# Optimization experiments

Hardware: AMD Instinct MI355X
Metric: run time of the kernel (lower is better)

The kernel has to match this reference:

```python
import jax, jax.numpy as jnp
import numpy as np

B, S, CC, CF, E, H, NH = 16, 1024, 8, 8, 64, 1024, 16
DH = H // NH
VOCAB = 10000
EPS = 1e-5


def layer_norm(x, g, b):
    m = x.mean(-1, keepdims=True)
    v = x.var(-1, keepdims=True)
    return (x - m) / jnp.sqrt(v + EPS) * g + b


def setup_inputs():
    key = jax.random.key(0)
    ks = jax.random.split(key, 30)
    f32 = jnp.float32
    n = lambda k, shp, s=0.02: jax.random.normal(k, shp, f32) * s
    inp = {}
    inp['cate_x'] = jax.random.randint(ks[0], (B, S, CC), 0, VOCAB)
    inp['cont_x'] = jax.random.normal(ks[1], (B, S, CF), f32)
    inp['mask'] = jax.random.randint(ks[2], (B, S), 0, 2)
    # parameters
    inp['emb_table'] = n(ks[3], (VOCAB, E)).at[0].set(0.0)  # padding_idx=0
    inp['cate_W'] = n(ks[4], (CC * E, H)); inp['cate_b'] = jnp.zeros((H,), f32)
    inp['cate_ln_g'] = jnp.ones((H,), f32); inp['cate_ln_b'] = jnp.zeros((H,), f32)
    inp['bn_g'] = jnp.ones((CF,), f32); inp['bn_b'] = jnp.zeros((CF,), f32)
    inp['cont_W'] = n(ks[5], (CF, H)); inp['cont_b'] = jnp.zeros((H,), f32)
    inp['cont_ln_g'] = jnp.ones((H,), f32); inp['cont_ln_b'] = jnp.zeros((H,), f32)
    inp['comb_W'] = n(ks[6], (2 * H, H)); inp['comb_b'] = jnp.zeros((H,), f32)
    inp['comb_ln_g'] = jnp.ones((H,), f32); inp['comb_ln_b'] = jnp.zeros((H,), f32)
    inp['Wq'] = n(ks[7], (H, H)); inp['bq'] = jnp.zeros((H,), f32)
    inp['Wk'] = n(ks[8], (H, H)); inp['bk'] = jnp.zeros((H,), f32)
    inp['Wv'] = n(ks[9], (H, H)); inp['bv'] = jnp.zeros((H,), f32)
    inp['Wo'] = n(ks[10], (H, H)); inp['bo'] = jnp.zeros((H,), f32)
    return inp


def reference(cate_x, cont_x, mask, emb_table, cate_W, cate_b, cate_ln_g, cate_ln_b,
              bn_g, bn_b, cont_W, cont_b, cont_ln_g, cont_ln_b,
              comb_W, comb_b, comb_ln_g, comb_ln_b,
              Wq, bq, Wk, bk, Wv, bv, Wo, bo):
    # categorical path: embed -> flatten cols -> Linear+LN
    cate_emb = emb_table[cate_x].reshape(B, S, CC * E)
    cate_h = layer_norm(cate_emb @ cate_W + cate_b, cate_ln_g, cate_ln_b)
    # continuous path: BatchNorm1d over flattened (B*S, CF) with batch stats
    xf = cont_x.reshape(-1, CF)
    mu = xf.mean(0)
    var = xf.var(0)  # biased, as torch BN normalization
    xn = ((xf - mu) / jnp.sqrt(var + EPS) * bn_g + bn_b).reshape(B, S, CF)
    cont_h = layer_norm(xn @ cont_W + cont_b, cont_ln_g, cont_ln_b)
    # combine: ReLU -> Linear -> LN
    seq = jax.nn.relu(jnp.concatenate([cate_h, cont_h], axis=2))
    x = layer_norm(seq @ comb_W + comb_b, comb_ln_g, comb_ln_b)  # [B,S,H]
    # multi-head attention (dropout is identity in eval)
    Q = (x @ Wq + bq).reshape(B, S, NH, DH)
    K = (x @ Wk + bk).reshape(B, S, NH, DH)
    V = (x @ Wv + bv).reshape(B, S, NH, DH)
    scores = jnp.einsum('bqhd,bkhd->bhqk', Q, K) / np.sqrt(DH).astype(np.float32)
    # faithful to source: mask broadcast over the QUERY axis
    scores = jnp.where(mask[:, None, :, None] == 0, -1e7, scores)
    attn = jax.nn.softmax(scores, axis=-1)
    out = jnp.einsum('bhqk,bkhd->bqhd', attn, V).reshape(B, S, H)
    out = out @ Wo + bo
    return out[:, -1:, -1]  # [B,1]
```

## Files before the change

kernel.cpp:

```cpp
#include <hip/hip_runtime.h>
#include <hip/hip_bf16.h>
#include <math.h>

#define EPS 1e-5f

typedef unsigned short u16;
typedef __attribute__((ext_vector_type(8))) short bf16x8;
typedef __attribute__((ext_vector_type(4))) float f32x4;

__device__ __forceinline__ float b2f(u16 u) {
  union { unsigned int i; float f; } v; v.i = ((unsigned int)u) << 16; return v.f;
}
__device__ __forceinline__ u16 f2b(float f) {
  union { float f; unsigned int i; } v; v.f = f;
  unsigned int r = v.i + 0x7fff + ((v.i >> 16) & 1);
  return (u16)(r >> 16);
}

__device__ __forceinline__ void gload_lds16(const u16* g, u16* l) {
  __builtin_amdgcn_global_load_lds(
      (const __attribute__((address_space(1))) unsigned int*)g,
      (__attribute__((address_space(3))) unsigned int*)l, 16, 0, 0);
}

__global__ __launch_bounds__(256) void prep_k(
    const float* __restrict__ cx, float* __restrict__ part_bn,
    float* __restrict__ out, float* __restrict__ Sall,
    const float* __restrict__ emb, u16* __restrict__ embb,
    const float* __restrict__ cate_W, u16* __restrict__ cateWT) {
  __shared__ float shmem[64 * 65];
  const int bid = blockIdx.x, tid = threadIdx.x;

  if (bid == 0) {
    if (tid < 16) out[tid] = 0.f;
    for (int i = tid; i < 544; i += 256) Sall[i] = 0.f;
    return;
  }
  if (bid <= 64) {
    int pb = bid - 1;
    int gid = pb * 256 + tid;
    float4 a = ((const float4*)cx)[2 * gid];
    float4 b = ((const float4*)cx)[2 * gid + 1];
    float v[16];
    v[0] = a.x; v[1] = a.y; v[2] = a.z; v[3] = a.w;
    v[4] = b.x; v[5] = b.y; v[6] = b.z; v[7] = b.w;
#pragma unroll
    for (int i = 0; i < 8; ++i) v[8 + i] = v[i] * v[i];
#pragma unroll
    for (int off = 32; off; off >>= 1)
#pragma unroll
      for (int i = 0; i < 16; ++i) v[i] += __shfl_down(v[i], off);
    int l = tid & 63, wv_ = tid >> 6;
    if (l == 0)
#pragma unroll
      for (int i = 0; i < 16; ++i) shmem[wv_ * 16 + i] = v[i];
    __syncthreads();
    if (tid < 16)
      part_bn[pb * 16 + tid] = shmem[tid] + shmem[16 + tid] + shmem[32 + tid] + shmem[48 + tid];
    return;
  }
  if (bid <= 689) {
    int i = (bid - 65) * 256 + tid;
    if (i < 160000) {
      float4 v = ((const float4*)emb)[i];
      ushort4 u; u.x = f2b(v.x); u.y = f2b(v.y); u.z = f2b(v.z); u.w = f2b(v.w);
      ((ushort4*)embb)[i] = u;
    }
    return;
  }
  {
    int local = bid - 690;
    int n0 = (local & 15) * 64, k0 = (local >> 4) * 64;
    int c = tid & 63, r0 = tid >> 6;
#pragma unroll
    for (int i = 0; i < 16; ++i) {
      int r = r0 + i * 4;
      shmem[r * 65 + c] = cate_W[(size_t)(k0 + r) * 1024 + n0 + c];
    }
    __syncthreads();
#pragma unroll
    for (int i = 0; i < 16; ++i) {
      int r = r0 + i * 4;
      cateWT[(size_t)(n0 + r) * 512 + k0 + c] = f2b(shmem[c * 65 + r]);
    }
  }
}

template <int MODE>
__global__ __launch_bounds__(512) void gemm256(
    const u16* __restrict__ A0, const u16* __restrict__ A1,
    const int* __restrict__ idx, const u16* __restrict__ embb,
    const u16* __restrict__ BT, const float* __restrict__ bias,
    u16* __restrict__ C, int K) {
  __shared__ u16 As[2][2][8192];
  __shared__ u16 Bs[2][2][8192];
  __shared__ int sidx[MODE == 1 ? 2048 : 4];
  const int tid = threadIdx.x;
  const int bid = blockIdx.x;
  const int chunk = gridDim.x >> 3;
  const int swz = (bid & 7) * chunk + (bid >> 3);
  const int row0 = (swz >> 2) * 256;
  const int col0 = (swz & 3) * 256;

  const int rr8 = tid >> 3;
  const int p8  = tid & 7;
  const int sl  = p8 ^ (rr8 & 7);

  const int l   = tid & 63;
  const int w   = tid >> 6;
  const int wrh = w >> 2;
  const int wcq = w & 3;
  const int hb  = wcq >> 1;
  const int rbb = (wcq & 1) * 64;
  const int lr  = l & 15;
  const int lk  = l >> 4;

  f32x4 acc[8][4];
#pragma unroll
  for (int m = 0; m < 8; ++m)
#pragma unroll
    for (int n = 0; n < 4; ++n) acc[m][n] = (f32x4){0.f, 0.f, 0.f, 0.f};

  const int nt = K >> 6;
  const int nit = nt >> 1;

  if (MODE == 1) {
    *(int4*)&sidx[tid * 4] = *(const int4*)&idx[row0 * 8 + tid * 4];
    __syncthreads();
  }

  auto stageA = [&](int t, int h) {
    const int k0 = t << 6;
    const int buf = t & 1;
#pragma unroll
    for (int i = 0; i < 2; ++i) {
      const u16* asrc;
      if (MODE == 1) {
        int id = sidx[(h * 128 + i * 64 + rr8) * 8 + (k0 >> 6)];
        asrc = embb + (size_t)id * 64 + sl * 8;
      } else {
        int ar = row0 + h * 128 + i * 64 + rr8;
        const u16* base = (k0 < 1024) ? A0 : A1;
        asrc = base + (size_t)ar * 1024 + (k0 & 1023) + sl * 8;
      }
      gload_lds16(asrc, &As[buf][h][i * 4096 + tid * 8]);
    }
  };
  auto stageB = [&](int t, int h) {
    const int k0 = t << 6;
    const int buf = t & 1;
#pragma unroll
    for (int i = 0; i < 2; ++i) {
      int br = col0 + h * 128 + i * 64 + rr8;
      gload_lds16(BT + (size_t)br * K + k0 + sl * 8,
                  &Bs[buf][h][i * 4096 + tid * 8]);
    }
  };

  bf16x8 bfr[4][2];
  auto loadB = [&](int buf) {
#pragma unroll
    for (int n = 0; n < 4; ++n)
#pragma unroll
      for (int ks = 0; ks < 2; ++ks) {
        int rowb = rbb + n * 16 + lr;
        int ph = (ks * 4 + lk) ^ (lr & 7);
        bfr[n][ks] = *(const bf16x8*)&Bs[buf][hb][rowb * 64 + ph * 8];
      }
  };
  auto loadA = [&](bf16x8 (&af)[2][2], int buf, int q) {
#pragma unroll
    for (int mm = 0; mm < 2; ++mm)
#pragma unroll
      for (int ks = 0; ks < 2; ++ks) {
        int rowa = (q * 2 + mm) * 16 + lr;
        int ph = (ks * 4 + lk) ^ (lr & 7);
        af[mm][ks] = *(const bf16x8*)&As[buf][wrh][rowa * 64 + ph * 8];
      }
  };
  auto mfma_quad = [&](bf16x8 (&af)[2][2], int q) {
    __builtin_amdgcn_s_setprio(1);
#pragma unroll
    for (int ks = 0; ks < 2; ++ks)
#pragma unroll
      for (int mm = 0; mm < 2; ++mm)
#pragma unroll
        for (int n = 0; n < 4; ++n)
          acc[q * 2 + mm][n] = __builtin_amdgcn_mfma_f32_16x16x32_bf16(
              af[mm][ks], bfr[n][ks], acc[q * 2 + mm][n], 0, 0, 0);
    __builtin_amdgcn_s_setprio(0);
  };

  stageA(0, 0); stageA(0, 1);
  stageB(0, 0); stageB(0, 1);
  stageB(1, 0); stageB(1, 1);
  asm volatile("s_waitcnt vmcnt(4)" ::: "memory");
  __builtin_amdgcn_s_barrier();

  for (int it = 0; it < nit; ++it) {
    const int T = it * 2;
    const bool more = (T + 2 < nt);
    bf16x8 af[2][2];

    loadB(0); loadA(af, 0, 0);
    stageA(T + 1, 0);
    __builtin_amdgcn_s_barrier();
    asm volatile("s_waitcnt lgkmcnt(0)" ::: "memory");
    mfma_quad(af, 0);
    __builtin_amdgcn_s_barrier();
    loadA(af, 0, 1);
    stageA(T + 1, 1);
    __builtin_amdgcn_s_barrier();
    asm volatile("s_waitcnt lgkmcnt(0)" ::: "memory");
    mfma_quad(af, 1);
    __builtin_amdgcn_s_barrier();
    loadA(af, 0, 2);
    if (more) stageB(T + 2, 0);
    __builtin_amdgcn_s_barrier();
    asm volatile("s_waitcnt lgkmcnt(0)" ::: "memory");
    mfma_quad(af, 2);
    __builtin_amdgcn_s_barrier();
    loadA(af, 0, 3);
    if (more) stageB(T + 2, 1);
    __builtin_amdgcn_s_barrier();
    asm volatile("s_waitcnt lgkmcnt(0)" ::: "memory");
    mfma_quad(af, 3);
    if (more) asm volatile("s_waitcnt vmcnt(4)" ::: "memory");
    else      asm volatile("s_waitcnt vmcnt(0)" ::: "memory");
    __builtin_amdgcn_s_barrier();

    loadB(1); loadA(af, 1, 0);
    if (more) stageA(T + 2, 0);
    __builtin_amdgcn_s_barrier();
    asm volatile("s_waitcnt lgkmcnt(0)" ::: "memory");
    mfma_quad(af, 0);
    __builtin_amdgcn_s_barrier();
    loadA(af, 1, 1);
    if (more) stageA(T + 2, 1);
    __builtin_amdgcn_s_barrier();
    asm volatile("s_waitcnt lgkmcnt(0)" ::: "memory");
    mfma_quad(af, 1);
    __builtin_amdgcn_s_barrier();
    loadA(af, 1, 2);
    if (more) stageB(T + 3, 0);
    __builtin_amdgcn_s_barrier();
    asm volatile("s_waitcnt lgkmcnt(0)" ::: "memory");
    mfma_quad(af, 2);
    __builtin_amdgcn_s_barrier();
    loadA(af, 1, 3);
    if (more) stageB(T + 3, 1);
    __builtin_amdgcn_s_barrier();
    asm volatile("s_waitcnt lgkmcnt(0)" ::: "memory");
    mfma_quad(af, 3);
    if (it + 1 < nit) {
      asm volatile("s_waitcnt vmcnt(4)" ::: "memory");
      __builtin_amdgcn_s_barrier();
    }
  }

  float bv_[4];
#pragma unroll
  for (int n = 0; n < 4; ++n) bv_[n] = bias[col0 + wcq * 64 + n * 16 + lr];
#pragma unroll
  for (int m = 0; m < 8; ++m) {
#pragma unroll
    for (int n = 0; n < 4; ++n) {
      int cc = col0 + wcq * 64 + n * 16 + lr;
#pragma unroll
      for (int q4 = 0; q4 < 4; ++q4) {
        int rr = row0 + wrh * 128 + m * 16 + lk * 4 + q4;
        C[(size_t)rr * 1024 + cc] = f2b(acc[m][n][q4] + bv_[n]);
      }
    }
  }
}

__device__ __forceinline__ void ln_body(u16* __restrict__ buf,
                                        const float* __restrict__ g,
                                        const float* __restrict__ b, int relu,
                                        int blk, int tid) {
  int lane = tid & 63, wave = tid >> 6;
  size_t row = (size_t)blk * 4 + wave;
  u16* p = buf + row * 1024 + lane * 16;
  uint4 u0 = *(uint4*)p;
  uint4 u1 = *(uint4*)(p + 8);
  float x[16];
#pragma unroll
  for (int i = 0; i < 4; ++i) {
    unsigned int w0 = ((unsigned int*)&u0)[i];
    unsigned int w1 = ((unsigned int*)&u1)[i];
    x[2 * i]     = b2f((u16)(w0 & 0xffff));
    x[2 * i + 1] = b2f((u16)(w0 >> 16));
    x[8 + 2 * i]     = b2f((u16)(w1 & 0xffff));
    x[8 + 2 * i + 1] = b2f((u16)(w1 >> 16));
  }
  float s = 0.f, s2 = 0.f;
#pragma unroll
  for (int i = 0; i < 16; ++i) { s += x[i]; s2 += x[i] * x[i]; }
#pragma unroll
  for (int off = 32; off; off >>= 1) { s += __shfl_xor(s, off); s2 += __shfl_xor(s2, off); }
  float mean = s * (1.f / 1024.f);
  float var = s2 * (1.f / 1024.f) - mean * mean;
  float rs = rsqrtf(var + EPS);
  float y[16];
#pragma unroll
  for (int q = 0; q < 4; ++q) {
    float4 gv = *(const float4*)(g + lane * 16 + q * 4);
    float4 bv = *(const float4*)(b + lane * 16 + q * 4);
    y[4 * q]     = (x[4 * q]     - mean) * rs * gv.x + bv.x;
    y[4 * q + 1] = (x[4 * q + 1] - mean) * rs * gv.y + bv.y;
    y[4 * q + 2] = (x[4 * q + 2] - mean) * rs * gv.z + bv.z;
    y[4 * q + 3] = (x[4 * q + 3] - mean) * rs * gv.w + bv.w;
  }
  if (relu)
#pragma unroll
    for (int i = 0; i < 16; ++i) y[i] = fmaxf(y[i], 0.f);
  uint4 o0, o1;
#pragma unroll
  for (int i = 0; i < 4; ++i) {
    ((unsigned int*)&o0)[i] = (unsigned int)f2b(y[2 * i]) | ((unsigned int)f2b(y[2 * i + 1]) << 16);
    ((unsigned int*)&o1)[i] = (unsigned int)f2b(y[8 + 2 * i]) | ((unsigned int)f2b(y[8 + 2 * i + 1]) << 16);
  }
  *(uint4*)p = o0;
  *(uint4*)(p + 8) = o1;
}

__device__ __forceinline__ void cont_body(const float* __restrict__ cx,
                                          const float* __restrict__ part_bn,
                                          const float* __restrict__ bn_g,
                                          const float* __restrict__ bn_b,
                                          const float* __restrict__ W,
                                          const float* __restrict__ cb,
                                          const float* __restrict__ g,
                                          const float* __restrict__ bb,
                                          u16* __restrict__ out,
                                          int row0, int tid) {
  __shared__ float sp[4][16];
  __shared__ float tt[16];
  __shared__ float ab[2][8];
  __shared__ float xn[8][8];
  __shared__ float rr1[4][8], rr2[4][8];

  if (tid < 64) {
    int f = tid & 15, qd = tid >> 4;
    float s = 0.f;
    for (int j = qd * 16; j < qd * 16 + 16; ++j) s += part_bn[j * 16 + f];
    sp[qd][f] = s;
  }
  __syncthreads();
  if (tid < 16) tt[tid] = sp[0][tid] + sp[1][tid] + sp[2][tid] + sp[3][tid];
  __syncthreads();
  if (tid < 8) {
    float mu = tt[tid] * (1.f / 16384.f);
    float var = tt[8 + tid] * (1.f / 16384.f) - mu * mu;
    float a = rsqrtf(var + EPS) * bn_g[tid];
    ab[0][tid] = a;
    ab[1][tid] = bn_b[tid] - mu * a;
  }
  __syncthreads();
  if (tid < 64) {
    int r = tid >> 3, f = tid & 7;
    xn[r][f] = ab[0][f] * cx[(row0 + r) * 8 + f] + ab[1][f];
  }
  __syncthreads();

  int c = tid * 4;
  float4 cbv = *(const float4*)(cb + c);
  float acc[8][4];
#pragma unroll
  for (int r = 0; r < 8; ++r) {
    acc[r][0] = cbv.x; acc[r][1] = cbv.y; acc[r][2] = cbv.z; acc[r][3] = cbv.w;
  }
  for (int k = 0; k < 8; ++k) {
    float4 w4 = *(const float4*)(W + k * 1024 + c);
#pragma unroll
    for (int r = 0; r < 8; ++r) {
      float xv = xn[r][k];
      acc[r][0] = fmaf(xv, w4.x, acc[r][0]);
      acc[r][1] = fmaf(xv, w4.y, acc[r][1]);
      acc[r][2] = fmaf(xv, w4.z, acc[r][2]);
      acc[r][3] = fmaf(xv, w4.w, acc[r][3]);
    }
  }
  float s1[8], s2[8];
#pragma unroll
  for (int r = 0; r < 8; ++r) {
    s1[r] = acc[r][0] + acc[r][1] + acc[r][2] + acc[r][3];
    s2[r] = acc[r][0] * acc[r][0] + acc[r][1] * acc[r][1] +
            acc[r][2] * acc[r][2] + acc[r][3] * acc[r][3];
  }
#pragma unroll
  for (int off = 32; off; off >>= 1)
#pragma unroll
    for (int r = 0; r < 8; ++r) {
      s1[r] += __shfl_down(s1[r], off);
      s2[r] += __shfl_down(s2[r], off);
    }
  int lane = tid & 63, wv = tid >> 6;
  if (lane == 0)
#pragma unroll
    for (int r = 0; r < 8; ++r) { rr1[wv][r] = s1[r]; rr2[wv][r] = s2[r]; }
  __syncthreads();
  float4 gv = *(const float4*)(g + c);
  float4 bv = *(const float4*)(bb + c);
#pragma unroll
  for (int r = 0; r < 8; ++r) {
    float ss = rr1[0][r] + rr1[1][r] + rr1[2][r] + rr1[3][r];
    float qq = rr2[0][r] + rr2[1][r] + rr2[2][r] + rr2[3][r];
    float mean = ss * (1.f / 1024.f);
    float var = qq * (1.f / 1024.f) - mean * mean;
    float rs = rsqrtf(var + EPS);
    float y0 = fmaxf((acc[r][0] - mean) * rs * gv.x + bv.x, 0.f);
    float y1 = fmaxf((acc[r][1] - mean) * rs * gv.y + bv.y, 0.f);
    float y2 = fmaxf((acc[r][2] - mean) * rs * gv.z + bv.z, 0.f);
    float y3 = fmaxf((acc[r][3] - mean) * rs * gv.w + bv.w, 0.f);
    ushort4 o; o.x = f2b(y0); o.y = f2b(y1); o.z = f2b(y2); o.w = f2b(y3);
    *(ushort4*)(out + (size_t)(row0 + r) * 1024 + c) = o;
  }
}

__global__ __launch_bounds__(256) void mid_k(
    u16* __restrict__ X1, const float* __restrict__ cate_g,
    const float* __restrict__ cate_bb,
    const float* __restrict__ comb_W, u16* __restrict__ combWT,
    const float* __restrict__ Wv, const float* __restrict__ Wo,
    const float* __restrict__ comb_g, const float* __restrict__ comb_bbv,
    u16* __restrict__ wvob_hi, u16* __restrict__ wvob_lo,
    float* __restrict__ Swg, float* __restrict__ Swb,
    const float* __restrict__ bv, const float* __restrict__ bo,
    float* __restrict__ bc,
    const float* __restrict__ cx, const float* __restrict__ part_bn,
    const float* __restrict__ bn_g, const float* __restrict__ bn_b,
    const float* __restrict__ cont_W, const float* __restrict__ cont_b,
    const float* __restrict__ cont_g, const float* __restrict__ cont_bb,
    u16* __restrict__ X2) {
  __shared__ float shmem[64 * 65];
  const int bid = blockIdx.x, tid = threadIdx.x;
  if (bid < 4096) {
    ln_body(X1, cate_g, cate_bb, 1, bid, tid);
    return;
  }
  if (bid < 4608) {
    int local = bid - 4096;
    int n0 = (local & 15) * 64, k0 = (local >> 4) * 64;
    int c = tid & 63, r0 = tid >> 6;
#pragma unroll
    for (int i = 0; i < 16; ++i) {
      int r = r0 + i * 4;
      shmem[r * 65 + c] = comb_W[(size_t)(k0 + r) * 1024 + n0 + c];
    }
    __syncthreads();
#pragma unroll
    for (int i = 0; i < 16; ++i) {
      int r = r0 + i * 4;
      combWT[(size_t)(n0 + r) * 2048 + k0 + c] = f2b(shmem[c * 65 + r]);
    }
    return;
  }
  if (bid < 4672) {
    int local = bid - 4608;
    int h = local >> 2, jc = local & 3;
    if (tid < 64) shmem[tid] = Wo[(size_t)(h * 64 + tid) * 1024 + 1023];
    __syncthreads();
    int j = jc * 256 + tid;
    const float* vr = Wv + (size_t)j * 1024 + h * 64;
    float s = 0.f;
    for (int d4 = 0; d4 < 64; d4 += 4) {
      float4 w4 = *(const float4*)(vr + d4);
      s = fmaf(w4.x, shmem[d4], s);
      s = fmaf(w4.y, shmem[d4 + 1], s);
      s = fmaf(w4.z, shmem[d4 + 2], s);
      s = fmaf(w4.w, shmem[d4 + 3], s);
    }
    float sg_ = s * comb_g[j];
    u16 hi = f2b(sg_);
    float lo = sg_ - b2f(hi);
    wvob_hi[h * 1024 + j] = hi;
    wvob_lo[h * 1024 + j] = f2b(lo);
    float swgp = sg_;
    float swbp = s * comb_bbv[j];
#pragma unroll
    for (int off = 32; off; off >>= 1) {
      swgp += __shfl_down(swgp, off);
      swbp += __shfl_down(swbp, off);
    }
    int lane = tid & 63, wv = tid >> 6;
    if (lane == 0) { shmem[64 + wv] = swgp; shmem[68 + wv] = swbp; }
    __syncthreads();
    if (tid == 0) {
      atomicAdd(&Swg[h], shmem[64] + shmem[65] + shmem[66] + shmem[67]);
      atomicAdd(&Swb[h], shmem[68] + shmem[69] + shmem[70] + shmem[71]);
    }
    return;
  }
  if (bid < 6720) {
    int row0 = (bid - 4672) * 8;
    cont_body(cx, part_bn, bn_g, bn_b, cont_W, cont_b, cont_g, cont_bb, X2,
              row0, tid);
    return;
  }
  {
    float s = 0.f;
    for (int i = tid; i < 1024; i += 256)
      s = fmaf(bv[i], Wo[(size_t)i * 1024 + 1023], s);
#pragma unroll
    for (int off = 32; off; off >>= 1) s += __shfl_down(s, off);
    int lane = tid & 63, wv = tid >> 6;
    if (lane == 0) shmem[wv] = s;
    __syncthreads();
    if (tid == 0) bc[0] = shmem[0] + shmem[1] + shmem[2] + shmem[3] + bo[1023];
  }
}

__global__ __launch_bounds__(256) void qproj_k(const u16* __restrict__ x,
                                               const float* __restrict__ g,
                                               const float* __restrict__ bb,
                                               const float* __restrict__ Wq,
                                               const float* __restrict__ bq,
                                               float* __restrict__ qpart) {
  __shared__ u16 xs[16][1024];
  __shared__ float part[16][16][16];
  __shared__ float ps1[16][16], ps2[16][16];
  __shared__ float sm[16], sr[16];
  int tid = threadIdx.x;
  int cb = blockIdx.x >> 2, kq4 = blockIdx.x & 3;
  for (int i = tid; i < 4096; i += 256) {
    int b = i >> 8, off = (i & 255) * 4;
    *(ushort4*)&xs[b][off] =
        *(const ushort4*)(x + ((size_t)(b * 1024 + 1023)) * 1024 + off);
  }
  __syncthreads();
  {
    int b = tid >> 4, seg = tid & 15;
    float s = 0.f, s2 = 0.f;
    for (int k = seg * 64; k < seg * 64 + 64; ++k) {
      float v = b2f(xs[b][k]);
      s += v;
      s2 = fmaf(v, v, s2);
    }
    ps1[b][seg] = s;
    ps2[b][seg] = s2;
  }
  __syncthreads();
  if (tid < 16) {
    float s = 0.f, s2 = 0.f;
#pragma unroll
    for (int j = 0; j < 16; ++j) { s += ps1[tid][j]; s2 += ps2[tid][j]; }
    float mean = s * (1.f / 1024.f);
    float var = s2 * (1.f / 1024.f) - mean * mean;
    sm[tid] = mean;
    sr[tid] = rsqrtf(var + EPS);
  }
  __syncthreads();
  for (int i = tid; i < 4096; i += 256) {
    int b = i >> 8, off = (i & 255) * 4;
    ushort4 u = *(ushort4*)&xs[b][off];
    float4 gv = *(const float4*)(g + off);
    float4 bvv = *(const float4*)(bb + off);
    float m = sm[b], r = sr[b];
    ushort4 o;
    o.x = f2b((b2f(u.x) - m) * r * gv.x + bvv.x);
    o.y = f2b((b2f(u.y) - m) * r * gv.y + bvv.y);
    o.z = f2b((b2f(u.z) - m) * r * gv.z + bvv.z);
    o.w = f2b((b2f(u.w) - m) * r * gv.w + bvv.w);
    *(ushort4*)&xs[b][off] = o;
  }
  __syncthreads();
  int c = tid & 15;
  int col = cb * 16 + c;
  int kq = tid >> 4;
  float acc[16];
#pragma unroll
  for (int b = 0; b < 16; ++b) acc[b] = 0.f;
  int kbase = kq4 * 256 + kq * 16;
  for (int k = kbase; k < kbase + 16; ++k) {
    float wv = Wq[(size_t)k * 1024 + col];
#pragma unroll
    for (int b = 0; b < 16; ++b) acc[b] = fmaf(b2f(xs[b][k]), wv, acc[b]);
  }
#pragma unroll
  for (int b = 0; b < 16; ++b) part[kq][b][c] = acc[b];
  __syncthreads();
  {
    int b = tid >> 4, cc = tid & 15;
    float s = 0.f;
#pragma unroll
    for (int j = 0; j < 16; ++j) s += part[j][b][cc];
    if (kq4 == 0) s += bq[cb * 16 + cc];
    qpart[kq4 * 16384 + b * 1024 + cb * 16 + cc] = s;
  }
}

__global__ __launch_bounds__(256) void kq_k(const float* __restrict__ Wk,
                                            const float* __restrict__ bk,
                                            const float* __restrict__ qpart,
                                            const float* __restrict__ g,
                                            const float* __restrict__ bb,
                                            u16* __restrict__ qtb,
                                            float* __restrict__ bkq,
                                            float* __restrict__ Sg,
                                            float* __restrict__ Sb) {
  int h = blockIdx.x >> 2, jc = blockIdx.x & 3;
  int tid = threadIdx.x;
  __shared__ float Qs[16][64];
  __shared__ float rg[4][16], rb[4][16];
  for (int i = tid; i < 1024; i += 256) {
    int b = i >> 6, d = i & 63;
    int o = b * 1024 + h * 64 + d;
    Qs[b][d] = qpart[o] + qpart[16384 + o] + qpart[32768 + o] + qpart[49152 + o];
  }
  __syncthreads();
  int j = jc * 256 + tid;
  float acc[16];
#pragma unroll
  for (int b = 0; b < 16; ++b) acc[b] = 0.f;
  const float* wr = Wk + (size_t)j * 1024 + h * 64;
  for (int d4 = 0; d4 < 64; d4 += 4) {
    float4 w4 = *(const float4*)(wr + d4);
#pragma unroll
    for (int b = 0; b < 16; ++b) {
      acc[b] = fmaf(w4.x, Qs[b][d4], acc[b]);
      acc[b] = fmaf(w4.y, Qs[b][d4 + 1], acc[b]);
      acc[b] = fmaf(w4.z, Qs[b][d4 + 2], acc[b]);
      acc[b] = fmaf(w4.w, Qs[b][d4 + 3], acc[b]);
    }
  }
  float gj = g[j], bbj = bb[j];
  float sgp[16], sbp[16];
#pragma unroll
  for (int b = 0; b < 16; ++b) {
    u16 qg = f2b(acc[b] * gj);
    qtb[((size_t)b * 16 + h) * 1024 + j] = qg;
    sgp[b] = b2f(qg);
    sbp[b] = acc[b] * bbj;
  }
#pragma unroll
  for (int off = 32; off; off >>= 1)
#pragma unroll
    for (int b = 0; b < 16; ++b) {
      sgp[b] += __shfl_down(sgp[b], off);
      sbp[b] += __shfl_down(sbp[b], off);
    }
  int lane = tid & 63, wv = tid >> 6;
  if (lane == 0)
#pragma unroll
    for (int b = 0; b < 16; ++b) { rg[wv][b] = sgp[b]; rb[wv][b] = sbp[b]; }
  __syncthreads();
  if (tid < 16) {
    int b = tid;
    atomicAdd(&Sg[b * 16 + h], rg[0][b] + rg[1][b] + rg[2][b] + rg[3][b]);
    atomicAdd(&Sb[b * 16 + h], rb[0][b] + rb[1][b] + rb[2][b] + rb[3][b]);
  }
  if (jc == 0 && tid < 16) {
    int b = tid;
    float s = 0.f;
    for (int d = 0; d < 64; ++d) s = fmaf(bk[h * 64 + d], Qs[b][d], s);
    bkq[b * 16 + h] = s;
  }
}

__global__ __launch_bounds__(256) void score_k(
    const u16* __restrict__ x, const u16* __restrict__ qtb,
    const float* __restrict__ bkq, const int* __restrict__ mask,
    const u16* __restrict__ whi, const u16* __restrict__ wlo,
    const float* __restrict__ Sg, const float* __restrict__ Sb,
    const float* __restrict__ Swg, const float* __restrict__ Swb,
    float* __restrict__ sc, float* __restrict__ y) {
  int b = blockIdx.x >> 6, kg = blockIdx.x & 63;
  int tid = threadIdx.x;
  int l = tid & 63, w = tid >> 6;
  int keybase = kg * 16;
  int lr = l & 15, ls = l >> 4;
  int masked = (mask[b * 1024 + 1023] == 0);

  bf16x8 ones;
#pragma unroll
  for (int j = 0; j < 8; ++j) ones[j] = (short)0x3F80;

  f32x4 acc = (f32x4){0.f, 0.f, 0.f, 0.f};
  f32x4 acy = (f32x4){0.f, 0.f, 0.f, 0.f};
  f32x4 as1 = (f32x4){0.f, 0.f, 0.f, 0.f};
  f32x4 as2 = (f32x4){0.f, 0.f, 0.f, 0.f};
  const u16* xb = x + (size_t)b * 1024 * 1024;
  const u16* qb = qtb + (size_t)b * 16 * 1024;
  const int k0beg = w * 256;
  for (int k0 = k0beg; k0 < k0beg + 256; k0 += 32) {
    bf16x8 bfr = *(const bf16x8*)&qb[(size_t)lr * 1024 + k0 + ls * 8];
    bf16x8 bh  = *(const bf16x8*)&whi[(size_t)lr * 1024 + k0 + ls * 8];
    bf16x8 bl  = *(const bf16x8*)&wlo[(size_t)lr * 1024 + k0 + ls * 8];
    bf16x8 afr = *(const bf16x8*)&xb[(size_t)(keybase + lr) * 1024 + k0 + ls * 8];
    acc = __builtin_amdgcn_mfma_f32_16x16x32_bf16(afr, bfr, acc, 0, 0, 0);
    acy = __builtin_amdgcn_mfma_f32_16x16x32_bf16(afr, bh, acy, 0, 0, 0);
    acy = __builtin_amdgcn_mfma_f32_16x16x32_bf16(afr, bl, acy, 0, 0, 0);
    as1 = __builtin_amdgcn_mfma_f32_16x16x32_bf16(afr, ones, as1, 0, 0, 0);
    as2 = __builtin_amdgcn_mfma_f32_16x16x32_bf16(afr, afr, as2, 0, 0, 0);
  }

  __shared__ float red[3][64][16];
  if (w > 0) {
    float* r = red[w - 1][l];
#pragma unroll
    for (int q = 0; q < 4; ++q) {
      r[q] = acc[q]; r[4 + q] = acy[q]; r[8 + q] = as1[q]; r[12 + q] = as2[q];
    }
  }
  __syncthreads();
  if (w == 0) {
#pragma unroll
    for (int i = 0; i < 3; ++i) {
      const float* r = red[i][l];
#pragma unroll
      for (int q = 0; q < 4; ++q) {
        acc[q] += r[q]; acy[q] += r[4 + q]; as1[q] += r[8 + q]; as2[q] += r[12 + q];
      }
    }
    int h = lr;
    float bq_  = bkq[b * 16 + h];
    float Sgv  = Sg[b * 16 + h];
    float Sbv  = Sb[b * 16 + h];
    float Swgv = Swg[h];
    float Swbv = Swb[h];
#pragma unroll
    for (int q = 0; q < 4; ++q) {
      int key = keybase + ls * 4 + q;
      float s1 = as1[q];
      float s2 = __shfl(as2[q], ls * 4 + q + 16 * ls);
      float mean = s1 * (1.f / 1024.f);
      float var  = s2 * (1.f / 1024.f) - mean * mean;
      float rs   = rsqrtf(var + EPS);
      float sraw = rs * acc[q] - rs * mean * Sgv + Sbv + bq_;
      float v = masked ? 0.f : sraw * 0.125f;
      sc[((size_t)b * 16 + h) * 1024 + key] = v;
      y[((size_t)b * 16 + h) * 1024 + key] =
          rs * acy[q] - rs * mean * Swgv + Swbv;
    }
  }
}

__global__ __launch_bounds__(256) void fin_k(const float* __restrict__ sc,
                                             const float* __restrict__ y,
                                             const float* __restrict__ bc,
                                             float* __restrict__ out) {
  int bh = blockIdx.x, tid = threadIdx.x;
  float4 v = ((const float4*)(sc + (size_t)bh * 1024))[tid];
  float m = fmaxf(fmaxf(v.x, v.y), fmaxf(v.z, v.w));
#pragma unroll
  for (int off = 32; off; off >>= 1) m = fmaxf(m, __shfl_down(m, off));
  __shared__ float rm[4], rs_[4], rd_[4];
  int lane = tid & 63, wv = tid >> 6;
  if (lane == 0) rm[wv] = m;
  __syncthreads();
  m = fmaxf(fmaxf(rm[0], rm[1]), fmaxf(rm[2], rm[3]));
  float e0 = expf(v.x - m), e1 = expf(v.y - m), e2 = expf(v.z - m), e3 = expf(v.w - m);
  float4 yv = ((const float4*)(y + (size_t)bh * 1024))[tid];
  float s = e0 + e1 + e2 + e3;
  float d = e0 * yv.x + e1 * yv.y + e2 * yv.z + e3 * yv.w;
#pragma unroll
  for (int off = 32; off; off >>= 1) {
    s += __shfl_down(s, off);
    d += __shfl_down(d, off);
  }
  if (lane == 0) { rs_[wv] = s; rd_[wv] = d; }
  __syncthreads();
  if (tid == 0) {
    float Z = rs_[0] + rs_[1] + rs_[2] + rs_[3];
    float D = rd_[0] + rd_[1] + rd_[2] + rd_[3];
    float add = D / Z;
    if ((bh & 15) == 0) add += bc[0];
    atomicAdd(&out[bh >> 4], add);
  }
}

extern "C" void kernel_launch(void* const* d_in, const int* in_sizes, int n_in,
                              void* d_out, int out_size, void* d_ws, size_t ws_size,
                              hipStream_t stream) {
  const int*   cate_x  = (const int*)d_in[0];
  const float* cont_x  = (const float*)d_in[1];
  const int*   mask    = (const int*)d_in[2];
  const float* emb     = (const float*)d_in[3];
  const float* cate_W  = (const float*)d_in[4];
  const float* cate_b  = (const float*)d_in[5];
  const float* cate_g  = (const float*)d_in[6];
  const float* cate_bb = (const float*)d_in[7];
  const float* bn_g    = (const float*)d_in[8];
  const float* bn_b    = (const float*)d_in[9];
  const float* cont_W  = (const float*)d_in[10];
  const float* cont_b  = (const float*)d_in[11];
  const float* cont_g  = (const float*)d_in[12];
  const float* cont_bb = (const float*)d_in[13];
  const float* Wq = (const float*)d_in[18]; const float* bq = (const float*)d_in[19];
  const float* Wk = (const float*)d_in[20]; const float* bk = (const float*)d_in[21];
  const float* Wv = (const float*)d_in[22]; const float* bv = (const float*)d_in[23];
  const float* Wo = (const float*)d_in[24]; const float* bo = (const float*)d_in[25];
  const float* comb_W  = (const float*)d_in[14];
  const float* comb_b  = (const float*)d_in[15];
  const float* comb_g  = (const float*)d_in[16];
  const float* comb_bb = (const float*)d_in[17];
  float* out = (float*)d_out;

  char* w = (char*)d_ws;
  float* part_bn = (float*)(w + 256);
  u16* embb      = (u16*)(w + 131328);
  u16* cateWT    = (u16*)(w + 1411328);
  u16* combWT    = (u16*)(w + 2459904);
  float* sc      = (float*)(w + 6654208);
  u16*   qtb     = (u16*)(w + 7702784);
  float* bkq     = (float*)(w + 8292608);
  float* ybuf    = (float*)(w + 8388608);
  u16* wvob_hi   = (u16*)(w + 9437184);
  u16* wvob_lo   = (u16*)(w + 9469952);
  float* qpart   = (float*)(w + 9506816);
  float* Sall    = (float*)(w + 10162176);
  float* Sg      = Sall;
  float* Sb      = Sall + 256;
  float* Swg     = Sall + 512;
  float* Swb     = Sall + 528;
  float* bc      = Sall + 552;
  u16* X1        = (u16*)(w + 10848512);
  u16* X2        = X1 + (size_t)16777216;
  u16* xb        = X2 + (size_t)16777216;

  prep_k<<<818, 256, 0, stream>>>(cont_x, part_bn, out, Sall, emb, embb,
                                  cate_W, cateWT);

  gemm256<1><<<256, 512, 0, stream>>>(nullptr, nullptr, cate_x, embb, cateWT,
                                      cate_b, X1, 512);
  mid_k<<<6721, 256, 0, stream>>>(X1, cate_g, cate_bb, comb_W, combWT, Wv, Wo,
                                  comb_g, comb_bb, wvob_hi, wvob_lo, Swg, Swb,
                                  bv, bo, bc, cont_x, part_bn, bn_g, bn_b,
                                  cont_W, cont_b, cont_g, cont_bb, X2);
  gemm256<2><<<256, 512, 0, stream>>>(X1, X2, nullptr, nullptr, combWT,
                                      comb_b, xb, 2048);

  qproj_k<<<256, 256, 0, stream>>>(xb, comb_g, comb_bb, Wq, bq, qpart);
  kq_k<<<64, 256, 0, stream>>>(Wk, bk, qpart, comb_g, comb_bb, qtb, bkq, Sg, Sb);
  score_k<<<1024, 256, 0, stream>>>(xb, qtb, bkq, mask, wvob_hi, wvob_lo,
                                    Sg, Sb, Swg, Swb, sc, ybuf);
  fin_k<<<256, 256, 0, stream>>>(sc, ybuf, bc, out);
}
```

Before: 181.5 us.

## Pre-gather embeddings into dense bf16 matrix before categorical GEMM

Replaces whole-table bf16 conversion and in-GEMM indexed gather with a separate kernel that gathers and converts the embedding rows for every token into a dense A matrix stored in the X2 buffer. The categorical GEMM then loads A contiguously instead of via shared-memory indices. This makes GEMM loads regular but adds a large extra write and read of the gathered activations in place of reading a small cached table.

```diff
diff --git a/kernel.cpp b/kernel.cpp
--- a/kernel.cpp
+++ b/kernel.cpp
@@ -23,10 +23,27 @@
       (__attribute__((address_space(3))) unsigned int*)l, 16, 0, 0);
 }
 
+__global__ __launch_bounds__(256) void gather_k(const int* __restrict__ idx,
+                                                const float* __restrict__ emb,
+                                                u16* __restrict__ Agath) {
+  int tid = threadIdx.x;
+  int p = blockIdx.x * 32 + (tid >> 3);
+  int q = tid & 7;
+  int id = idx[p];
+  const float* src = emb + (size_t)id * 64 + q * 8;
+  float4 a = *(const float4*)src;
+  float4 b = *(const float4*)(src + 4);
+  uint4 o;
+  o.x = (unsigned int)f2b(a.x) | ((unsigned int)f2b(a.y) << 16);
+  o.y = (unsigned int)f2b(a.z) | ((unsigned int)f2b(a.w) << 16);
+  o.z = (unsigned int)f2b(b.x) | ((unsigned int)f2b(b.y) << 16);
+  o.w = (unsigned int)f2b(b.z) | ((unsigned int)f2b(b.w) << 16);
+  *(uint4*)(Agath + (size_t)p * 64 + q * 8) = o;
+}
+
 __global__ __launch_bounds__(256) void prep_k(
     const float* __restrict__ cx, float* __restrict__ part_bn,
     float* __restrict__ out, float* __restrict__ Sall,
-    const float* __restrict__ emb, u16* __restrict__ embb,
     const float* __restrict__ cate_W, u16* __restrict__ cateWT) {
   __shared__ float shmem[64 * 65];
   const int bid = blockIdx.x, tid = threadIdx.x;
@@ -59,17 +76,8 @@
       part_bn[pb * 16 + tid] = shmem[tid] + shmem[16 + tid] + shmem[32 + tid] + shmem[48 + tid];
     return;
   }
-  if (bid <= 689) {
-    int i = (bid - 65) * 256 + tid;
-    if (i < 160000) {
-      float4 v = ((const float4*)emb)[i];
-      ushort4 u; u.x = f2b(v.x); u.y = f2b(v.y); u.z = f2b(v.z); u.w = f2b(v.w);
-      ((ushort4*)embb)[i] = u;
-    }
-    return;
-  }
   {
-    int local = bid - 690;
+    int local = bid - 65;
     int n0 = (local & 15) * 64, k0 = (local >> 4) * 64;
     int c = tid & 63, r0 = tid >> 6;
 #pragma unroll
@@ -89,12 +97,10 @@
 template <int MODE>
 __global__ __launch_bounds__(512) void gemm256(
     const u16* __restrict__ A0, const u16* __restrict__ A1,
-    const int* __restrict__ idx, const u16* __restrict__ embb,
     const u16* __restrict__ BT, const float* __restrict__ bias,
     u16* __restrict__ C, int K) {
   __shared__ u16 As[2][2][8192];
   __shared__ u16 Bs[2][2][8192];
-  __shared__ int sidx[MODE == 1 ? 2048 : 4];
   const int tid = threadIdx.x;
   const int bid = blockIdx.x;
   const int chunk = gridDim.x >> 3;
@@ -124,22 +130,16 @@
   const int nt = K >> 6;
   const int nit = nt >> 1;
 
-  if (MODE == 1) {
-    *(int4*)&sidx[tid * 4] = *(const int4*)&idx[row0 * 8 + tid * 4];
-    __syncthreads();
-  }
-
   auto stageA = [&](int t, int h) {
     const int k0 = t << 6;
     const int buf = t & 1;
 #pragma unroll
     for (int i = 0; i < 2; ++i) {
+      int ar = row0 + h * 128 + i * 64 + rr8;
       const u16* asrc;
       if (MODE == 1) {
-        int id = sidx[(h * 128 + i * 64 + rr8) * 8 + (k0 >> 6)];
-        asrc = embb + (size_t)id * 64 + sl * 8;
+        asrc = A0 + (size_t)ar * 512 + k0 + sl * 8;
       } else {
-        int ar = row0 + h * 128 + i * 64 + rr8;
         const u16* base = (k0 < 1024) ? A0 : A1;
         asrc = base + (size_t)ar * 1024 + (k0 & 1023) + sl * 8;
       }
@@ -800,7 +800,6 @@
 
   char* w = (char*)d_ws;
   float* part_bn = (float*)(w + 256);
-  u16* embb      = (u16*)(w + 131328);
   u16* cateWT    = (u16*)(w + 1411328);
   u16* combWT    = (u16*)(w + 2459904);
   float* sc      = (float*)(w + 6654208);
@@ -819,18 +818,17 @@
   u16* X1        = (u16*)(w + 10848512);
   u16* X2        = X1 + (size_t)16777216;
   u16* xb        = X2 + (size_t)16777216;
-
-  prep_k<<<818, 256, 0, stream>>>(cont_x, part_bn, out, Sall, emb, embb,
-                                  cate_W, cateWT);
-
-  gemm256<1><<<256, 512, 0, stream>>>(nullptr, nullptr, cate_x, embb, cateWT,
-                                      cate_b, X1, 512);
+  u16* Agath     = X2;
+
+  gather_k<<<4096, 256, 0, stream>>>(cate_x, emb, Agath);
+  prep_k<<<193, 256, 0, stream>>>(cont_x, part_bn, out, Sall, cate_W, cateWT);
+
+  gemm256<1><<<256, 512, 0, stream>>>(Agath, nullptr, cateWT, cate_b, X1, 512);
   mid_k<<<6721, 256, 0, stream>>>(X1, cate_g, cate_bb, comb_W, combWT, Wv, Wo,
                                   comb_g, comb_bb, wvob_hi, wvob_lo, Swg, Swb,
                                   bv, bo, bc, cont_x, part_bn, bn_g, bn_b,
                                   cont_W, cont_b, cont_g, cont_bb, X2);
-  gemm256<2><<<256, 512, 0, stream>>>(X1, X2, nullptr, nullptr, combWT,
-                                      comb_b, xb, 2048);
+  gemm256<2><<<256, 512, 0, stream>>>(X1, X2, combWT, comb_b, xb, 2048);
 
   qproj_k<<<256, 256, 0, stream>>>(xb, comb_g, comb_bb, Wq, bq, qpart);
   kq_k<<<64, 256, 0, stream>>>(Wk, bk, qpart, comb_g, comb_bb, qtb, bkq, Sg, Sb);
```

After: 185.7 us. 2.3% more time.

## Fuse last-token Q projection and K-fold kernels into one launch

Applied to the files above, without the earlier changes.

Merges qproj_k and kq_k into a single qk_k kernel. Each of the 64 blocks (one head, one column quarter) computes the head's 64 Q columns over all of K and reduces the four partial sums in shared memory, so the qpart buffer round trip and one kernel launch go away. In exchange each head's Q slice is recomputed by 4 blocks, and the grid falls from 256 to 64 blocks, each running a longer serial 256-step K loop per thread. That lowers parallelism and adds redundant Wq reads.

```diff
diff --git a/kernel.cpp b/kernel.cpp
--- a/kernel.cpp
+++ b/kernel.cpp
@@ -512,18 +512,26 @@
   }
 }
 
-__global__ __launch_bounds__(256) void qproj_k(const u16* __restrict__ x,
-                                               const float* __restrict__ g,
-                                               const float* __restrict__ bb,
-                                               const float* __restrict__ Wq,
-                                               const float* __restrict__ bq,
-                                               float* __restrict__ qpart) {
+__global__ __launch_bounds__(256) void qk_k(const u16* __restrict__ x,
+                                            const float* __restrict__ g,
+                                            const float* __restrict__ bb,
+                                            const float* __restrict__ Wq,
+                                            const float* __restrict__ bq,
+                                            const float* __restrict__ Wk,
+                                            const float* __restrict__ bk,
+                                            u16* __restrict__ qtb,
+                                            float* __restrict__ bkq,
+                                            float* __restrict__ Sg,
+                                            float* __restrict__ Sb) {
   __shared__ u16 xs[16][1024];
-  __shared__ float part[16][16][16];
+  __shared__ float part[4][16][64];
   __shared__ float ps1[16][16], ps2[16][16];
   __shared__ float sm[16], sr[16];
+  __shared__ float Qs[16][64];
+  __shared__ float rg[4][16], rb[4][16];
   int tid = threadIdx.x;
-  int cb = blockIdx.x >> 2, kq4 = blockIdx.x & 3;
+  int h = blockIdx.x >> 2, jc = blockIdx.x & 3;
+
   for (int i = tid; i < 4096; i += 256) {
     int b = i >> 8, off = (i & 255) * 4;
     *(ushort4*)&xs[b][off] =
@@ -566,50 +574,29 @@
     *(ushort4*)&xs[b][off] = o;
   }
   __syncthreads();
-  int c = tid & 15;
-  int col = cb * 16 + c;
-  int kq = tid >> 4;
-  float acc[16];
-#pragma unroll
-  for (int b = 0; b < 16; ++b) acc[b] = 0.f;
-  int kbase = kq4 * 256 + kq * 16;
-  for (int k = kbase; k < kbase + 16; ++k) {
-    float wv = Wq[(size_t)k * 1024 + col];
-#pragma unroll
-    for (int b = 0; b < 16; ++b) acc[b] = fmaf(b2f(xs[b][k]), wv, acc[b]);
-  }
-#pragma unroll
-  for (int b = 0; b < 16; ++b) part[kq][b][c] = acc[b];
-  __syncthreads();
   {
-    int b = tid >> 4, cc = tid & 15;
-    float s = 0.f;
-#pragma unroll
-    for (int j = 0; j < 16; ++j) s += part[j][b][cc];
-    if (kq4 == 0) s += bq[cb * 16 + cc];
-    qpart[kq4 * 16384 + b * 1024 + cb * 16 + cc] = s;
-  }
-}
-
-__global__ __launch_bounds__(256) void kq_k(const float* __restrict__ Wk,
-                                            const float* __restrict__ bk,
-                                            const float* __restrict__ qpart,
-                                            const float* __restrict__ g,
-                                            const float* __restrict__ bb,
-                                            u16* __restrict__ qtb,
-                                            float* __restrict__ bkq,
-                                            float* __restrict__ Sg,
-                                            float* __restrict__ Sb) {
-  int h = blockIdx.x >> 2, jc = blockIdx.x & 3;
-  int tid = threadIdx.x;
-  __shared__ float Qs[16][64];
-  __shared__ float rg[4][16], rb[4][16];
+    int c = tid & 63;
+    int kq = tid >> 6;
+    int col = h * 64 + c;
+    float acc[16];
+#pragma unroll
+    for (int b = 0; b < 16; ++b) acc[b] = 0.f;
+    for (int k = kq * 256; k < kq * 256 + 256; ++k) {
+      float wv = Wq[(size_t)k * 1024 + col];
+#pragma unroll
+      for (int b = 0; b < 16; ++b) acc[b] = fmaf(b2f(xs[b][k]), wv, acc[b]);
+    }
+#pragma unroll
+    for (int b = 0; b < 16; ++b) part[kq][b][c] = acc[b];
+  }
+  __syncthreads();
   for (int i = tid; i < 1024; i += 256) {
     int b = i >> 6, d = i & 63;
-    int o = b * 1024 + h * 64 + d;
-    Qs[b][d] = qpart[o] + qpart[16384 + o] + qpart[32768 + o] + qpart[49152 + o];
-  }
-  __syncthreads();
+    Qs[b][d] = part[0][b][d] + part[1][b][d] + part[2][b][d] + part[3][b][d] +
+               bq[h * 64 + d];
+  }
+  __syncthreads();
+
   int j = jc * 256 + tid;
   float acc[16];
 #pragma unroll
@@ -809,7 +796,6 @@
   float* ybuf    = (float*)(w + 8388608);
   u16* wvob_hi   = (u16*)(w + 9437184);
   u16* wvob_lo   = (u16*)(w + 9469952);
-  float* qpart   = (float*)(w + 9506816);
   float* Sall    = (float*)(w + 10162176);
   float* Sg      = Sall;
   float* Sb      = Sall + 256;
@@ -832,8 +818,8 @@
   gemm256<2><<<256, 512, 0, stream>>>(X1, X2, nullptr, nullptr, combWT,
                                       comb_b, xb, 2048);
 
-  qproj_k<<<256, 256, 0, stream>>>(xb, comb_g, comb_bb, Wq, bq, qpart);
-  kq_k<<<64, 256, 0, stream>>>(Wk, bk, qpart, comb_g, comb_bb, qtb, bkq, Sg, Sb);
+  qk_k<<<64, 256, 0, stream>>>(xb, comb_g, comb_bb, Wq, bq, Wk, bk, qtb, bkq,
+                               Sg, Sb);
   score_k<<<1024, 256, 0, stream>>>(xb, qtb, bkq, mask, wvob_hi, wvob_lo,
                                     Sg, Sb, Swg, Swb, sc, ybuf);
   fin_k<<<256, 256, 0, stream>>>(sc, ybuf, bc, out);
```

Result: slower. 208.3 us (+14.8%).
